# Kernel tuning notes

Hardware: AMD Instinct MI355X
Metric: run time of the kernel (lower is better)

Reference implementation:

```python
import jax, jax.numpy as jnp
import numpy as np

B, S, HID = 1, 2048, 2048
H, NOPE, ROPE, VDIM = 16, 128, 64, 128
QR, KVR = 1536, 512
IH, ID = 16, 128
TOPK = 512
THETA = 10000.0
EPS = 1e-6
SCALE = (NOPE + ROPE) ** -0.5
NEG = -1e9


def _cos_sin(s, dim, dtype):
    inv = 1.0 / (THETA ** (np.arange(0, dim, 2, dtype=np.float32) / dim))
    t = np.arange(s, dtype=np.float32)
    f = np.outer(t, inv)
    emb = np.concatenate([f, f], -1)
    return jnp.asarray(np.cos(emb), dtype), jnp.asarray(np.sin(emb), dtype)


def _rope(x, cos, sin):
    # x: [b,s,h,d]; cos/sin: [s,d]; NeoX-style rotate_half
    x1, x2 = jnp.split(x, 2, axis=-1)
    rot = jnp.concatenate([-x2, x1], axis=-1)
    return x * cos[None, :, None, :] + rot * sin[None, :, None, :]


def _rmsnorm(x, w):
    v = jnp.mean(x.astype(jnp.float32) ** 2, -1, keepdims=True)
    return (x.astype(jnp.float32) * jax.lax.rsqrt(v + EPS)).astype(x.dtype) * w


def _layernorm(x, w, b):
    m = jnp.mean(x, -1, keepdims=True)
    v = jnp.var(x, -1, keepdims=True)
    return (x - m) * jax.lax.rsqrt(v + EPS) * w + b


def setup_inputs() -> dict:
    key = jax.random.key(0)
    ks = jax.random.split(key, 12)
    g = lambda k, shp: jax.random.normal(k, shp, jnp.float32) * 0.02
    return {
        'hidden_states': jax.random.normal(ks[0], (B, S, HID), jnp.float32),
        'q_a_w': g(ks[1], (QR, HID)),
        'q_a_ln_w': jnp.ones((QR,), jnp.float32),
        'q_b_w': g(ks[2], (H * (NOPE + ROPE), QR)),
        'kv_a_w': g(ks[3], (KVR + ROPE, HID)),
        'kv_a_ln_w': jnp.ones((KVR,), jnp.float32),
        'kv_b_w': g(ks[4], (H * (NOPE + VDIM), KVR)),
        'o_w': g(ks[5], (HID, H * VDIM)),
        'idx_wq_b_w': g(ks[6], (IH * ID, QR)),
        'idx_wk_w': g(ks[7], (ID, HID)),
        'idx_kn_w': jnp.ones((ID,), jnp.float32),
        'idx_kn_b': jnp.zeros((ID,), jnp.float32),
        'idx_wproj_w': g(ks[8], (IH, HID)),
    }


def reference(hidden_states, q_a_w, q_a_ln_w, q_b_w, kv_a_w, kv_a_ln_w, kv_b_w, o_w,
              idx_wq_b_w, idx_wk_w, idx_kn_w, idx_kn_b, idx_wproj_w):
    b, s, _ = hidden_states.shape
    cos, sin = _cos_sin(s, ROPE, hidden_states.dtype)

    # --- MLA projections ---
    qr = _rmsnorm(hidden_states @ q_a_w.T, q_a_ln_w)                 # [b,s,QR]
    q = (qr @ q_b_w.T).reshape(b, s, H, NOPE + ROPE)
    q_nope, q_pe = q[..., :NOPE], q[..., NOPE:]
    q_pe = _rope(q_pe, cos, sin)
    ckv = hidden_states @ kv_a_w.T                                   # [b,s,KVR+ROPE]
    c_kv, k_pe = ckv[..., :KVR], ckv[..., KVR:]
    k_pe = _rope(k_pe[:, :, None, :], cos, sin)                      # [b,s,1,ROPE]
    kv = (_rmsnorm(c_kv, kv_a_ln_w) @ kv_b_w.T).reshape(b, s, H, NOPE + VDIM)
    k_nope, v = kv[..., :NOPE], kv[..., NOPE:]

    # --- DSA indexer: per-token importance scores ---
    iq = (qr @ idx_wq_b_w.T).reshape(b, s, IH, ID)
    iq = jnp.concatenate([_rope(iq[..., :ROPE], cos, sin), iq[..., ROPE:]], -1)
    ik = _layernorm(hidden_states @ idx_wk_w.T, idx_kn_w, idx_kn_b)  # [b,s,ID]
    ik_pe = _rope(ik[:, :, None, :ROPE], cos, sin)[:, :, 0, :]
    ik = jnp.concatenate([ik_pe, ik[..., ROPE:]], -1)
    iw = (hidden_states @ idx_wproj_w.T) * (IH ** -0.5)              # [b,s,IH]
    idx_scores = jnp.einsum('bqh,bhqk->bqk', iw,
                            jax.nn.relu(jnp.einsum('bqhd,bkd->bhqk', iq, ik)))
    causal = jnp.tril(jnp.ones((s, s), bool))
    idx_scores = jnp.where(causal[None], idx_scores, -jnp.inf)
    _, top_idx = jax.lax.top_k(idx_scores, TOPK)                     # [b,s,TOPK]
    bi = jnp.arange(b)[:, None, None]
    qi = jnp.arange(s)[None, :, None]
    keep = jnp.zeros((b, s, s), bool).at[bi, qi, top_idx].set(True)
    allowed = keep & causal[None]                                    # [b,s,s]

    # --- sparse top-k attention (top-k mask to -inf before softmax) ---
    qh = jnp.concatenate([q_nope, q_pe], -1)                         # [b,s,H,192]
    kh = jnp.concatenate([k_nope, jnp.broadcast_to(k_pe, (b, s, H, ROPE))], -1)
    scores = jnp.einsum('bqhd,bkhd->bhqk', qh, kh) * SCALE
    scores = jnp.where(allowed[:, None], scores, NEG)
    attn = jax.nn.softmax(scores, -1)
    out = jnp.einsum('bhqk,bkhd->bqhd', attn, v).reshape(b, s, H * VDIM)
    return out @ o_w.T
```

## Files before the change

kernel.cpp:

```cpp
#include <hip/hip_runtime.h>
#include <hip/hip_bf16.h>
#include <math.h>

#define SEQ 2048
#define HIDD 2048
#define QRANK 1536
#define KVRANK 512
#define TOPK 512
#define EPSF 1e-6f
#define SCALE_ATTN 0.07216878364870323f
#define NCAT 1680

typedef __attribute__((ext_vector_type(8))) short short8v;
typedef __attribute__((ext_vector_type(4))) short short4v;
typedef __attribute__((ext_vector_type(4))) float f32x4;

__device__ inline unsigned short f2bf(float f) {
    unsigned u = __float_as_uint(f);
    unsigned r = (u + 0x7FFFu + ((u >> 16) & 1u)) >> 16;
    return (unsigned short)r;
}
__device__ inline float bf2f(unsigned short b) {
    return __uint_as_float(((unsigned)b) << 16);
}
__device__ inline void split2(float x, unsigned short& h, unsigned short& l) {
    h = f2bf(x);
    l = f2bf(x - bf2f(h));
}

__device__ inline short4v ds_read_tr16(const void* p) {
#if __has_builtin(__builtin_amdgcn_ds_read_tr16_b64)
    return __builtin_amdgcn_ds_read_tr16_b64((short4v*)p);
#else
    const unsigned short* u = (const unsigned short*)p;
    short4v r;
    r[0] = (short)u[0]; r[1] = (short)u[16]; r[2] = (short)u[32]; r[3] = (short)u[48];
    return r;
#endif
}

__global__ __launch_bounds__(256) void cvt_bf16_4_kernel(
    const float* __restrict__ a, int na4, const float* __restrict__ b, int nb4,
    const float* __restrict__ c, int nc4, const float* __restrict__ d, int nd4,
    unsigned short* __restrict__ oa, unsigned short* __restrict__ ob,
    unsigned short* __restrict__ oc, unsigned short* __restrict__ od,
    float* __restrict__ cos_t, float* __restrict__ sin_t)
{
    if (blockIdx.x < SEQ && threadIdx.x < 32) {
        int s = blockIdx.x, i = threadIdx.x;
        double inv = pow(10000.0, -((double)(2 * i)) / 64.0);
        double f = (double)s * inv;
        cos_t[s * 32 + i] = (float)cos(f);
        sin_t[s * 32 + i] = (float)sin(f);
    }
    int total = na4 + nb4 + nc4 + nd4;
    for (int i = blockIdx.x * 256 + threadIdx.x; i < total; i += gridDim.x * 256) {
        const float* src; unsigned short* dst; int j = i;
        if (j < na4) { src = a; dst = oa; }
        else if ((j -= na4) < nb4) { src = b; dst = ob; }
        else if ((j -= nb4) < nc4) { src = c; dst = oc; }
        else { j -= nc4; src = d; dst = od; }
        float4 v = ((const float4*)src)[j];
        ushort4 o;
        o.x = f2bf(v.x); o.y = f2bf(v.y); o.z = f2bf(v.z); o.w = f2bf(v.w);
        ((ushort4*)dst)[j] = o;
    }
}

__global__ __launch_bounds__(256) void cvt_split3_kernel(
    const float* __restrict__ hidden, const float* __restrict__ q_a_w,
    const float* __restrict__ idx_wk_w, const float* __restrict__ idx_wproj_w,
    const float* __restrict__ wq,
    unsigned short* __restrict__ hidh, unsigned short* __restrict__ hidl,
    unsigned short* __restrict__ catwh, unsigned short* __restrict__ catwl,
    unsigned short* __restrict__ wqh, unsigned short* __restrict__ wql)
{
    const int nhid4 = HIDD * HIDD / 4;
    const int ncat4 = NCAT * HIDD / 4;
    const int nwq4  = HIDD * QRANK / 4;
    int total = nhid4 + ncat4 + nwq4;
    for (int i = blockIdx.x * 256 + threadIdx.x; i < total; i += gridDim.x * 256) {
        int j = i;
        const float4* s4;
        unsigned short *dh, *dl;
        float scale = 1.f;
        if (j < nhid4) {
            s4 = (const float4*)hidden + j; dh = hidh; dl = hidl;
        } else if ((j -= nhid4) < ncat4) {
            int row = (j * 4) >> 11;
            dh = catwh; dl = catwl;
            if (row < 1536) s4 = (const float4*)q_a_w + j;
            else if (row < 1664) s4 = (const float4*)idx_wk_w + (j - 1536 * 512);
            else { s4 = (const float4*)idx_wproj_w + (j - 1664 * 512); scale = 0.25f; }
        } else {
            j -= ncat4;
            s4 = (const float4*)wq + j; dh = wqh; dl = wql;
        }
        float4 v = *s4;
        float xs[4] = {v.x * scale, v.y * scale, v.z * scale, v.w * scale};
        ushort4 oh, ol;
        unsigned short h2, l2;
        split2(xs[0], h2, l2); oh.x = h2; ol.x = l2;
        split2(xs[1], h2, l2); oh.y = h2; ol.y = l2;
        split2(xs[2], h2, l2); oh.z = h2; ol.z = l2;
        split2(xs[3], h2, l2); oh.w = h2; ol.w = l2;
        ((ushort4*)dh)[j] = oh;
        ((ushort4*)dl)[j] = ol;
    }
}

__global__ __launch_bounds__(256) void wkt_kernel(const float* __restrict__ kvb,
                                                  unsigned short* __restrict__ wkt) {
    __shared__ float t[128][129];
    int h = blockIdx.x, n0 = blockIdx.y * 128;
    int tid = threadIdx.x;
    for (int it = tid; it < 128 * 32; it += 256) {
        int d = it >> 5, c4 = it & 31;
        float4 v = *(const float4*)(kvb + ((size_t)(h * 256 + d)) * 512 + n0 + c4 * 4);
        t[d][c4 * 4 + 0] = v.x; t[d][c4 * 4 + 1] = v.y;
        t[d][c4 * 4 + 2] = v.z; t[d][c4 * 4 + 3] = v.w;
    }
    __syncthreads();
    for (int it = tid; it < 128 * 32; it += 256) {
        int n = it >> 5, dc = it & 31;
        ushort4 o;
        o.x = f2bf(t[dc * 4 + 0][n]); o.y = f2bf(t[dc * 4 + 1][n]);
        o.z = f2bf(t[dc * 4 + 2][n]); o.w = f2bf(t[dc * 4 + 3][n]);
        *(ushort4*)(wkt + ((size_t)h * 512 + n0 + n) * 128 + dc * 4) = o;
    }
}

__global__ __launch_bounds__(256) void gemm_cat_split_kernel(
    const float* __restrict__ hidden, const float* __restrict__ q_a_w,
    const float* __restrict__ idx_wk_w, const float* __restrict__ idx_wproj_w,
    const unsigned short* __restrict__ hidh, const unsigned short* __restrict__ hidl,
    const unsigned short* __restrict__ catwh, const unsigned short* __restrict__ catwl,
    float* __restrict__ ccat)
{
    __shared__ __align__(16) unsigned short Ah[128 * 32], Al[128 * 32];
    __shared__ __align__(16) unsigned short Bh[128 * 32], Bl[128 * 32];
    int tid = threadIdx.x;
    int l = tid & 63, w = tid >> 6;
    int wr = w >> 1, wc = w & 1;
    int m0 = blockIdx.x * 128, n0 = blockIdx.y * 128;
    const bool pre = (hidh != nullptr);
    f32x4 acc[4][4] = {};
    for (int k0 = 0; k0 < HIDD; k0 += 32) {
        __syncthreads();
#pragma unroll
        for (int i = 0; i < 2; ++i) {
            int idx = tid + i * 256;
            int r = idx >> 2, cc = idx & 3;
            int sw = cc ^ (r & 3);
            int gb = n0 + r; if (gb > NCAT - 1) gb = NCAT - 1;
            if (pre) {
                size_t abase = (size_t)(m0 + r) * HIDD + k0 + cc * 8;
                *(short8v*)&Ah[r * 32 + sw * 8] = *(const short8v*)(hidh + abase);
                *(short8v*)&Al[r * 32 + sw * 8] = *(const short8v*)(hidl + abase);
                size_t bbase = (size_t)gb * HIDD + k0 + cc * 8;
                *(short8v*)&Bh[r * 32 + sw * 8] = *(const short8v*)(catwh + bbase);
                *(short8v*)&Bl[r * 32 + sw * 8] = *(const short8v*)(catwl + bbase);
            } else {
                {
                    const float* src = hidden + (size_t)(m0 + r) * HIDD + k0 + cc * 8;
                    float4 f0 = *(const float4*)src, f1 = *(const float4*)(src + 4);
                    float xs[8] = {f0.x, f0.y, f0.z, f0.w, f1.x, f1.y, f1.z, f1.w};
                    short8v dh, dl;
#pragma unroll
                    for (int e = 0; e < 8; ++e) {
                        unsigned short hh, ll; split2(xs[e], hh, ll);
                        dh[e] = (short)hh; dl[e] = (short)ll;
                    }
                    *(short8v*)&Ah[r * 32 + sw * 8] = dh;
                    *(short8v*)&Al[r * 32 + sw * 8] = dl;
                }
                {
                    float scale = 1.f;
                    const float* src;
                    if (gb < 1536) src = q_a_w + (size_t)gb * HIDD;
                    else if (gb < 1664) src = idx_wk_w + (size_t)(gb - 1536) * HIDD;
                    else { src = idx_wproj_w + (size_t)(gb - 1664) * HIDD; scale = 0.25f; }
                    src += k0 + cc * 8;
                    float4 f0 = *(const float4*)src, f1 = *(const float4*)(src + 4);
                    float xs[8] = {f0.x, f0.y, f0.z, f0.w, f1.x, f1.y, f1.z, f1.w};
                    short8v dh, dl;
#pragma unroll
                    for (int e = 0; e < 8; ++e) {
                        unsigned short hh, ll; split2(xs[e] * scale, hh, ll);
                        dh[e] = (short)hh; dl[e] = (short)ll;
                    }
                    *(short8v*)&Bh[r * 32 + sw * 8] = dh;
                    *(short8v*)&Bl[r * 32 + sw * 8] = dl;
                }
            }
        }
        __syncthreads();
        short8v avh[4], avl[4];
#pragma unroll
        for (int mt = 0; mt < 4; ++mt) {
            int row = wr * 64 + mt * 16 + (l & 15);
            int ch = (l >> 4) ^ (row & 3);
            avh[mt] = *(const short8v*)&Ah[row * 32 + ch * 8];
            avl[mt] = *(const short8v*)&Al[row * 32 + ch * 8];
        }
#pragma unroll
        for (int nt = 0; nt < 4; ++nt) {
            int row = wc * 64 + nt * 16 + (l & 15);
            int ch = (l >> 4) ^ (row & 3);
            short8v bvh = *(const short8v*)&Bh[row * 32 + ch * 8];
            short8v bvl = *(const short8v*)&Bl[row * 32 + ch * 8];
#pragma unroll
            for (int mt = 0; mt < 4; ++mt) {
                acc[mt][nt] = __builtin_amdgcn_mfma_f32_16x16x32_bf16(avh[mt], bvh, acc[mt][nt], 0, 0, 0);
                acc[mt][nt] = __builtin_amdgcn_mfma_f32_16x16x32_bf16(avh[mt], bvl, acc[mt][nt], 0, 0, 0);
                acc[mt][nt] = __builtin_amdgcn_mfma_f32_16x16x32_bf16(avl[mt], bvh, acc[mt][nt], 0, 0, 0);
            }
        }
    }
#pragma unroll
    for (int mt = 0; mt < 4; ++mt)
#pragma unroll
        for (int nt = 0; nt < 4; ++nt)
#pragma unroll
            for (int i = 0; i < 4; ++i) {
                int gm = m0 + wr * 64 + mt * 16 + (l >> 4) * 4 + i;
                int gn = n0 + wc * 64 + nt * 16 + (l & 15);
                if (gn < NCAT) ccat[(size_t)gm * NCAT + gn] = acc[mt][nt][i];
            }
}

__global__ __launch_bounds__(256) void gemm_iq_split_kernel(
    const float* __restrict__ qr, const float* __restrict__ wq,
    const unsigned short* __restrict__ qrh, const unsigned short* __restrict__ qrl,
    const unsigned short* __restrict__ wqh, const unsigned short* __restrict__ wql,
    const float* __restrict__ cos_t, const float* __restrict__ sin_t,
    unsigned short* __restrict__ iqh, unsigned short* __restrict__ iql)
{
    __shared__ __align__(16) unsigned short Ah[128 * 32], Al[128 * 32];
    __shared__ __align__(16) unsigned short Bh[128 * 32], Bl[128 * 32];
    int tid = threadIdx.x;
    int l = tid & 63, w = tid >> 6;
    int wr = w >> 1, wc = w & 1;
    int m0 = blockIdx.x * 128, n0 = blockIdx.y * 128;
    int hh_ = blockIdx.y;
    const bool pre = (wqh != nullptr);
    f32x4 acc[4][4] = {};
    for (int k0 = 0; k0 < QRANK; k0 += 32) {
        __syncthreads();
#pragma unroll
        for (int i = 0; i < 2; ++i) {
            int idx = tid + i * 256;
            int r = idx >> 2, cc = idx & 3;
            int sw = cc ^ (r & 3);
            if (pre) {
                size_t abase = (size_t)(m0 + r) * QRANK + k0 + cc * 8;
                *(short8v*)&Ah[r * 32 + sw * 8] = *(const short8v*)(qrh + abase);
                *(short8v*)&Al[r * 32 + sw * 8] = *(const short8v*)(qrl + abase);
                size_t bbase = (size_t)(n0 + r) * QRANK + k0 + cc * 8;
                *(short8v*)&Bh[r * 32 + sw * 8] = *(const short8v*)(wqh + bbase);
                *(short8v*)&Bl[r * 32 + sw * 8] = *(const short8v*)(wql + bbase);
            } else {
                {
                    const float* src = qr + (size_t)(m0 + r) * QRANK + k0 + cc * 8;
                    float4 f0 = *(const float4*)src, f1 = *(const float4*)(src + 4);
                    float xs[8] = {f0.x, f0.y, f0.z, f0.w, f1.x, f1.y, f1.z, f1.w};
                    short8v dh, dl;
#pragma unroll
                    for (int e = 0; e < 8; ++e) {
                        unsigned short h2, l2; split2(xs[e], h2, l2);
                        dh[e] = (short)h2; dl[e] = (short)l2;
                    }
                    *(short8v*)&Ah[r * 32 + sw * 8] = dh;
                    *(short8v*)&Al[r * 32 + sw * 8] = dl;
                }
                {
                    const float* src = wq + (size_t)(n0 + r) * QRANK + k0 + cc * 8;
                    float4 f0 = *(const float4*)src, f1 = *(const float4*)(src + 4);
                    float xs[8] = {f0.x, f0.y, f0.z, f0.w, f1.x, f1.y, f1.z, f1.w};
                    short8v dh, dl;
#pragma unroll
                    for (int e = 0; e < 8; ++e) {
                        unsigned short h2, l2; split2(xs[e], h2, l2);
                        dh[e] = (short)h2; dl[e] = (short)l2;
                    }
                    *(short8v*)&Bh[r * 32 + sw * 8] = dh;
                    *(short8v*)&Bl[r * 32 + sw * 8] = dl;
                }
            }
        }
        __syncthreads();
        short8v avh[4], avl[4];
#pragma unroll
        for (int mt = 0; mt < 4; ++mt) {
            int row = wr * 64 + mt * 16 + (l & 15);
            int ch = (l >> 4) ^ (row & 3);
            avh[mt] = *(const short8v*)&Ah[row * 32 + ch * 8];
            avl[mt] = *(const short8v*)&Al[row * 32 + ch * 8];
        }
#pragma unroll
        for (int nt = 0; nt < 4; ++nt) {
            int row = wc * 64 + nt * 16 + (l & 15);
            int ch = (l >> 4) ^ (row & 3);
            short8v bvh = *(const short8v*)&Bh[row * 32 + ch * 8];
            short8v bvl = *(const short8v*)&Bl[row * 32 + ch * 8];
#pragma unroll
            for (int mt = 0; mt < 4; ++mt) {
                acc[mt][nt] = __builtin_amdgcn_mfma_f32_16x16x32_bf16(avh[mt], bvh, acc[mt][nt], 0, 0, 0);
                acc[mt][nt] = __builtin_amdgcn_mfma_f32_16x16x32_bf16(avh[mt], bvl, acc[mt][nt], 0, 0, 0);
                acc[mt][nt] = __builtin_amdgcn_mfma_f32_16x16x32_bf16(avl[mt], bvh, acc[mt][nt], 0, 0, 0);
            }
        }
    }
    if (wc == 0) {
#pragma unroll
        for (int mt = 0; mt < 4; ++mt)
#pragma unroll
            for (int nt = 0; nt < 2; ++nt)
#pragma unroll
                for (int i = 0; i < 4; ++i) {
                    int q = m0 + wr * 64 + mt * 16 + (l >> 4) * 4 + i;
                    int dd = nt * 16 + (l & 15);
                    float c = cos_t[q * 32 + dd], s = sin_t[q * 32 + dd];
                    float x1 = acc[mt][nt][i], x2 = acc[mt][nt + 2][i];
                    acc[mt][nt][i] = x1 * c - x2 * s;
                    acc[mt][nt + 2][i] = x2 * c + x1 * s;
                }
    }
#pragma unroll
    for (int mt = 0; mt < 4; ++mt)
#pragma unroll
        for (int nt = 0; nt < 4; ++nt)
#pragma unroll
            for (int i = 0; i < 4; ++i) {
                int q = m0 + wr * 64 + mt * 16 + (l >> 4) * 4 + i;
                int d = wc * 64 + nt * 16 + (l & 15);
                size_t idx = ((size_t)q * 16 + hh_) * 128 + d;
                unsigned short h2, l2; split2(acc[mt][nt][i], h2, l2);
                iqh[idx] = h2; iql[idx] = l2;
            }
}

template <typename TA, typename TC>
__global__ __launch_bounds__(256) void mfma_nt_kernel(
    const TA* __restrict__ A, const unsigned short* __restrict__ B, TC* __restrict__ C,
    int M, int N, int K, int lda, int ldb, int ldc, long ab, long bb, long cb,
    const float* __restrict__ cos_t, const float* __restrict__ sin_t, int rope_mode,
    unsigned short* __restrict__ qnope)
{
    __shared__ __align__(16) unsigned short Asl[128 * 32];
    __shared__ __align__(16) unsigned short Bsl[128 * 32];
    int z = blockIdx.z;
    const TA* Az = A + (size_t)z * ab;
    const unsigned short* Bz = B + (size_t)z * bb;
    TC* Cz = C + (size_t)z * cb;
    int tid = threadIdx.x;
    int l = tid & 63, w = tid >> 6;
    int wr = w >> 1, wc = w & 1;
    int m0 = blockIdx.x * 128, n0 = blockIdx.y * 128;
    f32x4 acc[4][4] = {};

    for (int k0 = 0; k0 < K; k0 += 32) {
        __syncthreads();
#pragma unroll
        for (int i = 0; i < 2; ++i) {
            int idx = tid + i * 256;
            int r = idx >> 2, cc = idx & 3;
            int sw = cc ^ (r & 3);
            {
                short8v d;
                const TA* src = Az + (size_t)(m0 + r) * lda + k0 + cc * 8;
                if constexpr (sizeof(TA) == 2) {
                    d = *(const short8v*)src;
                } else {
                    float4 f0 = *(const float4*)src;
                    float4 f1 = *(const float4*)(src + 4);
                    d[0] = (short)f2bf(f0.x); d[1] = (short)f2bf(f0.y);
                    d[2] = (short)f2bf(f0.z); d[3] = (short)f2bf(f0.w);
                    d[4] = (short)f2bf(f1.x); d[5] = (short)f2bf(f1.y);
                    d[6] = (short)f2bf(f1.z); d[7] = (short)f2bf(f1.w);
                }
                *(short8v*)&Asl[r * 32 + sw * 8] = d;
            }
            {
                int gb = n0 + r; if (gb > N - 1) gb = N - 1;
                short8v d = *(const short8v*)(Bz + (size_t)gb * ldb + k0 + cc * 8);
                *(short8v*)&Bsl[r * 32 + sw * 8] = d;
            }
        }
        __syncthreads();
        short8v av[4], bv[4];
#pragma unroll
        for (int mt = 0; mt < 4; ++mt) {
            int row = wr * 64 + mt * 16 + (l & 15);
            int ch = (l >> 4) ^ (row & 3);
            av[mt] = *(const short8v*)&Asl[row * 32 + ch * 8];
        }
#pragma unroll
        for (int nt = 0; nt < 4; ++nt) {
            int row = wc * 64 + nt * 16 + (l & 15);
            int ch = (l >> 4) ^ (row & 3);
            bv[nt] = *(const short8v*)&Bsl[row * 32 + ch * 8];
        }
#pragma unroll
        for (int mt = 0; mt < 4; ++mt)
#pragma unroll
            for (int nt = 0; nt < 4; ++nt)
                acc[mt][nt] = __builtin_amdgcn_mfma_f32_16x16x32_bf16(av[mt], bv[nt], acc[mt][nt], 0, 0, 0);
    }
    if (rope_mode) {
        int gcol64 = (n0 >> 6) + wc;
        bool dorope = (rope_mode == 1) ? ((gcol64 % 3) == 2) : (gcol64 == 8);
        if (dorope) {
#pragma unroll
            for (int mt = 0; mt < 4; ++mt)
#pragma unroll
                for (int nt = 0; nt < 2; ++nt)
#pragma unroll
                    for (int i = 0; i < 4; ++i) {
                        int q = m0 + wr * 64 + mt * 16 + (l >> 4) * 4 + i;
                        int dd = nt * 16 + (l & 15);
                        float c = cos_t[q * 32 + dd], sn = sin_t[q * 32 + dd];
                        float x1 = acc[mt][nt][i], x2 = acc[mt][nt + 2][i];
                        acc[mt][nt][i] = x1 * c - x2 * sn;
                        acc[mt][nt + 2][i] = x2 * c + x1 * sn;
                    }
        }
    }
#pragma unroll
    for (int mt = 0; mt < 4; ++mt) {
#pragma unroll
        for (int nt = 0; nt < 4; ++nt) {
#pragma unroll
            for (int i = 0; i < 4; ++i) {
                int gm = m0 + wr * 64 + mt * 16 + (l >> 4) * 4 + i;
                int gn = n0 + wc * 64 + nt * 16 + (l & 15);
                if (gn < N) {
                    float v = acc[mt][nt][i];
                    if constexpr (sizeof(TC) == 4) Cz[(size_t)gm * ldc + gn] = v;
                    else Cz[(size_t)gm * ldc + gn] = f2bf(v);
                    if (rope_mode == 1 && qnope) {
                        int gh = gn / 192, gr = gn - gh * 192;
                        if (gr < 128)
                            qnope[(size_t)gm * 2048 + gh * 128 + gr] = f2bf(v);
                    }
                }
            }
        }
    }
}

__global__ __launch_bounds__(256) void norms_fused_kernel(
    const float* __restrict__ ccat,
    const float* __restrict__ q_a_ln_w, float* __restrict__ qr_out,
    unsigned short* __restrict__ qr_bf, unsigned short* __restrict__ qr_lo,
    const float* __restrict__ ikn_w, const float* __restrict__ ikn_b,
    const float* __restrict__ cos_t, const float* __restrict__ sin_t,
    unsigned short* __restrict__ ikh, unsigned short* __restrict__ ikl)
{
    int blk = blockIdx.x, tid = threadIdx.x;
    if (blk < SEQ) {
        int row = blk;
        const float* x = ccat + (size_t)row * NCAT;
        float4 v[2];
        int cnt = 0;
        float ss = 0.f;
        const int nf4 = QRANK >> 2;
        for (int i = tid; i < nf4; i += 256) {
            float4 t = *(const float4*)(x + i * 4);
            v[cnt++] = t;
            ss += t.x * t.x + t.y * t.y + t.z * t.z + t.w * t.w;
        }
#pragma unroll
        for (int m = 32; m; m >>= 1) ss += __shfl_xor(ss, m);
        __shared__ float red[8];
        if ((tid & 63) == 0) red[tid >> 6] = ss;
        __syncthreads();
        if (tid == 0) {
            float s = red[0] + red[1] + red[2] + red[3];
            red[4] = rsqrtf(s / (float)QRANK + EPSF);
        }
        __syncthreads();
        float scale = red[4];
        cnt = 0;
        for (int i = tid; i < nf4; i += 256) {
            float4 t = v[cnt++];
            float4 wv = *(const float4*)(q_a_ln_w + i * 4);
            float4 o;
            o.x = t.x * scale * wv.x; o.y = t.y * scale * wv.y;
            o.z = t.z * scale * wv.z; o.w = t.w * scale * wv.w;
            *(float4*)(qr_out + (size_t)row * QRANK + i * 4) = o;
            ushort4 ob;
            ob.x = f2bf(o.x); ob.y = f2bf(o.y); ob.z = f2bf(o.z); ob.w = f2bf(o.w);
            *(ushort4*)(qr_bf + (size_t)row * QRANK + i * 4) = ob;
            if (qr_lo) {
                ushort4 ol;
                ol.x = f2bf(o.x - bf2f(ob.x)); ol.y = f2bf(o.y - bf2f(ob.y));
                ol.z = f2bf(o.z - bf2f(ob.z)); ol.w = f2bf(o.w - bf2f(ob.w));
                *(ushort4*)(qr_lo + (size_t)row * QRANK + i * 4) = ol;
            }
        }
    } else {
        if (tid >= 64) return;
        int row = blk - SEQ;
        const float* x = ccat + (size_t)row * NCAT + 1536;
        float x0 = x[tid], x1 = x[tid + 64];
        float s = x0 + x1, ss = x0 * x0 + x1 * x1;
#pragma unroll
        for (int m = 32; m; m >>= 1) { s += __shfl_xor(s, m); ss += __shfl_xor(ss, m); }
        float mean = s * (1.f / 128.f);
        float var = ss * (1.f / 128.f) - mean * mean;
        float r = rsqrtf(var + EPSF);
        float n0 = (x0 - mean) * r * ikn_w[tid] + ikn_b[tid];
        float n1 = (x1 - mean) * r * ikn_w[tid + 64] + ikn_b[tid + 64];
        float c = cos_t[row * 32 + (tid & 31)], sn = sin_t[row * 32 + (tid & 31)];
        float other = __shfl_xor(n0, 32);
        float r0 = (tid < 32) ? (n0 * c - other * sn) : (n0 * c + other * sn);
        unsigned short h2, l2;
        split2(r0, h2, l2);
        ikh[(size_t)row * 128 + tid] = h2; ikl[(size_t)row * 128 + tid] = l2;
        split2(n1, h2, l2);
        ikh[(size_t)row * 128 + 64 + tid] = h2; ikl[(size_t)row * 128 + 64 + tid] = l2;
    }
}

__global__ __launch_bounds__(256) void rmsnorm_khg_kernel(
    const float* __restrict__ ckv, const float* __restrict__ w,
    unsigned short* __restrict__ khg)
{
    int row = blockIdx.x, tid = threadIdx.x;
    const float* x = ckv + (size_t)row * 576;
    float4 v = make_float4(0.f, 0.f, 0.f, 0.f);
    float ss = 0.f;
    if (tid < 128) {
        v = *(const float4*)(x + tid * 4);
        ss = v.x * v.x + v.y * v.y + v.z * v.z + v.w * v.w;
    }
#pragma unroll
    for (int mm = 32; mm; mm >>= 1) ss += __shfl_xor(ss, mm);
    __shared__ float red[8];
    if ((tid & 63) == 0) red[tid >> 6] = ss;
    __syncthreads();
    if (tid == 0) red[4] = rsqrtf((red[0] + red[1] + red[2] + red[3]) * (1.f / 512.f) + EPSF);
    __syncthreads();
    float scale = red[4];
    if (tid < 128) {
        float4 wv = *(const float4*)(w + tid * 4);
        ushort4 ob;
        ob.x = f2bf(v.x * scale * wv.x); ob.y = f2bf(v.y * scale * wv.y);
        ob.z = f2bf(v.z * scale * wv.z); ob.w = f2bf(v.w * scale * wv.w);
        *(ushort4*)(khg + (size_t)row * 576 + tid * 4) = ob;
    } else if (tid < 192) {
        khg[(size_t)row * 576 + 512 + (tid - 128)] = f2bf(x[512 + tid - 128]);
    }
}

__global__ __launch_bounds__(256) void idx_scores_mfma_kernel(
    const unsigned short* __restrict__ iqh, const unsigned short* __restrict__ iql,
    const unsigned short* __restrict__ ikh, const unsigned short* __restrict__ ikl,
    const float* __restrict__ iwsrc, int iw_stride,
    float* __restrict__ scores)
{
    int q0 = blockIdx.x * 64, k0 = blockIdx.y * 64;
    int tid = threadIdx.x;
    if (k0 > q0 + 63) {
        for (int t = tid; t < 64 * 64; t += 256) {
            int r = t >> 6, c = t & 63;
            scores[(size_t)(q0 + r) * SEQ + k0 + c] = -INFINITY;
        }
        return;
    }
    __shared__ float iws[64][16];
    int l = tid & 63, w = tid >> 6;
    {
        int r = tid >> 2, c = tid & 3;
        *(float4*)&iws[r][c * 4] = *(const float4*)(iwsrc + (size_t)(q0 + r) * iw_stride + c * 4);
    }
    __syncthreads();
    short8v bhr[4][4], blr[4][4];
#pragma unroll
    for (int nt = 0; nt < 4; ++nt)
#pragma unroll
        for (int ks = 0; ks < 4; ++ks) {
            size_t base = (size_t)(k0 + nt * 16 + (l & 15)) * 128 + ks * 32 + (l >> 4) * 8;
            bhr[nt][ks] = *(const short8v*)(ikh + base);
            blr[nt][ks] = *(const short8v*)(ikl + base);
        }
    f32x4 acc[4] = {};
    const int arow = q0 + w * 16 + (l & 15);
    for (int h = 0; h < 16; ++h) {
        f32x4 dot[4] = {};
#pragma unroll
        for (int ks = 0; ks < 4; ++ks) {
            size_t abase = ((size_t)arow * 16 + h) * 128 + ks * 32 + (l >> 4) * 8;
            short8v ah = *(const short8v*)(iqh + abase);
            short8v al = *(const short8v*)(iql + abase);
#pragma unroll
            for (int nt = 0; nt < 4; ++nt) {
                dot[nt] = __builtin_amdgcn_mfma_f32_16x16x32_bf16(ah, bhr[nt][ks], dot[nt], 0, 0, 0);
                dot[nt] = __builtin_amdgcn_mfma_f32_16x16x32_bf16(ah, blr[nt][ks], dot[nt], 0, 0, 0);
                dot[nt] = __builtin_amdgcn_mfma_f32_16x16x32_bf16(al, bhr[nt][ks], dot[nt], 0, 0, 0);
            }
        }
#pragma unroll
        for (int nt = 0; nt < 4; ++nt)
#pragma unroll
            for (int i = 0; i < 4; ++i) {
                float wv = iws[w * 16 + (l >> 4) * 4 + i][h];
                acc[nt][i] += wv * fmaxf(dot[nt][i], 0.f);
            }
    }
#pragma unroll
    for (int nt = 0; nt < 4; ++nt)
#pragma unroll
        for (int i = 0; i < 4; ++i) {
            int q = q0 + w * 16 + (l >> 4) * 4 + i;
            int k = k0 + nt * 16 + (l & 15);
            scores[(size_t)q * SEQ + k] = (k <= q) ? acc[nt][i] : -INFINITY;
        }
}

__global__ __launch_bounds__(1024) void topk_kernel(
    const float* __restrict__ scores, int* __restrict__ sel)
{
    int qi = blockIdx.x, tid = threadIdx.x;
    __shared__ unsigned long long keys[2048];
    const float* srow = scores + (size_t)qi * SEQ;
#pragma unroll
    for (int r = 0; r < 2; ++r) {
        int k = tid + r * 1024;
        unsigned u = __float_as_uint(srow[k]);
        unsigned mv = (u & 0x80000000u) ? ~u : (u | 0x80000000u);
        keys[k] = ((unsigned long long)mv << 32) | (unsigned)(2047 - k);
    }
    for (int ksz = 2; ksz <= 2048; ksz <<= 1) {
        for (int j = ksz >> 1; j > 0; j >>= 1) {
            __syncthreads();
#pragma unroll 1
            for (int r = 0; r < 2; ++r) {
                int i = tid + r * 1024;
                int ixj = i ^ j;
                if (ixj > i) {
                    unsigned long long a = keys[i], b = keys[ixj];
                    bool dir = ((i & ksz) == 0);
                    if ((a < b) == dir) { keys[i] = b; keys[ixj] = a; }
                }
            }
        }
    }
    __syncthreads();
    if (tid < TOPK) {
        int k = 2047 - (int)(keys[tid] & 0xFFFFFFFFu);
        sel[(size_t)qi * TOPK + tid] = (tid <= qi) ? k : -1;
    }
}

__global__ __launch_bounds__(256) void attn_mfma_kernel(
    const unsigned short* __restrict__ qabs,
    const float* __restrict__ qsrc,
    const unsigned short* __restrict__ khg,
    const int* __restrict__ sel,
    unsigned short* __restrict__ ocomp)
{
    __shared__ __align__(16) char smem[77824];
    unsigned short* plds = (unsigned short*)(smem + 74752);
    float* smax = (float*)(smem + 77312);
    float* ssum = (float*)(smem + 77568);

    const int qi = blockIdx.x;
    const int tid = threadIdx.x;
    const int l = tid & 63, w = tid >> 6;
    const int lg = l >> 4, lr = l & 15;
    const int nv = min(TOPK, qi + 1);
    const int ntile = (nv + 63) >> 6;
    const int krow = w * 16 + lr;

    const int ck = tid >> 6, cc = tid & 63;
    const int pk = tid >> 3, pc = tid & 7;
    const int* selrow = sel + (size_t)qi * TOPK;

    short8v aq[18];
    {
        const unsigned short* qa = qabs + ((size_t)qi * 16 + lr) * 512 + lg * 8;
#pragma unroll
        for (int ks = 0; ks < 16; ++ks)
            aq[ks] = *(const short8v*)(qa + ks * 32);
        const float* qp = qsrc + (size_t)qi * 3072 + lr * 192 + 128 + lg * 8;
#pragma unroll
        for (int ks = 0; ks < 2; ++ks) {
            float4 f0 = *(const float4*)(qp + ks * 32);
            float4 f1 = *(const float4*)(qp + ks * 32 + 4);
            short8v d;
            d[0] = (short)f2bf(f0.x); d[1] = (short)f2bf(f0.y);
            d[2] = (short)f2bf(f0.z); d[3] = (short)f2bf(f0.w);
            d[4] = (short)f2bf(f1.x); d[5] = (short)f2bf(f1.y);
            d[6] = (short)f2bf(f1.z); d[7] = (short)f2bf(f1.w);
            aq[16 + ks] = d;
        }
    }

    const int sbase = krow * 32 + (lg >> 1) * 2080 + (lg & 1) * 16;
    const int vboff = w * 16640 + lg * 256 + lr * 2;

    float m[4] = {-1e30f, -1e30f, -1e30f, -1e30f};
    float lsum[4] = {0.f, 0.f, 0.f, 0.f};
    f32x4 oacc[8] = {};

    for (int t = 0; t < ntile; ++t) {
        const int j0 = t * 64;
        __syncthreads();
#pragma unroll
        for (int j = 0; j < 16; ++j) {
            int sv = selrow[j0 + ck + 4 * j];
            if (sv < 0) sv = 0;
            short8v v = *(const short8v*)(khg + (size_t)sv * 576 + cc * 8);
            *(short8v*)(smem + (cc >> 1) * 2080 + (ck + 4 * j) * 32 + (cc & 1) * 16) = v;
        }
#pragma unroll
        for (int j = 0; j < 2; ++j) {
            int sv = selrow[j0 + pk + 32 * j];
            if (sv < 0) sv = 0;
            short8v v = *(const short8v*)(khg + (size_t)sv * 576 + 512 + pc * 8);
            int key = pk + 32 * j;
            *(short8v*)(smem + 66560 + ((key * 128 + pc * 16) ^ ((key & 7) << 4))) = v;
        }
        __syncthreads();
        f32x4 s = {};
        __builtin_amdgcn_s_setprio(1);
#pragma unroll
        for (int ks = 0; ks < 16; ++ks) {
            short8v b = *(const short8v*)(smem + sbase + ks * 4160);
            s = __builtin_amdgcn_mfma_f32_16x16x32_bf16(aq[ks], b, s, 0, 0, 0);
        }
#pragma unroll
        for (int ks = 0; ks < 2; ++ks) {
            short8v b = *(const short8v*)(smem + 66560 +
                ((krow * 128 + ks * 64 + lg * 16) ^ ((krow & 7) << 4)));
            s = __builtin_amdgcn_mfma_f32_16x16x32_bf16(aq[16 + ks], b, s, 0, 0, 0);
        }
        __builtin_amdgcn_s_setprio(0);
        bool kvalid = (j0 + krow) < nv;
#pragma unroll
        for (int i = 0; i < 4; ++i)
            s[i] = kvalid ? s[i] * SCALE_ATTN : -1e30f;
        float tm[4];
#pragma unroll
        for (int i = 0; i < 4; ++i) tm[i] = s[i];
#pragma unroll
        for (int sh = 1; sh < 16; sh <<= 1)
#pragma unroll
            for (int i = 0; i < 4; ++i) tm[i] = fmaxf(tm[i], __shfl_xor(tm[i], sh));
        if (lr == 0) *(float4*)&smax[w * 16 + lg * 4] = make_float4(tm[0], tm[1], tm[2], tm[3]);
        __syncthreads();
        float mn[4], scl[4];
#pragma unroll
        for (int i = 0; i < 4; ++i) {
            int h = lg * 4 + i;
            float tmax = fmaxf(fmaxf(smax[h], smax[16 + h]), fmaxf(smax[32 + h], smax[48 + h]));
            mn[i] = fmaxf(m[i], tmax);
            scl[i] = __expf(m[i] - mn[i]);
            m[i] = mn[i];
        }
        float p[4], rs[4];
#pragma unroll
        for (int i = 0; i < 4; ++i) { p[i] = __expf(s[i] - mn[i]); rs[i] = p[i]; }
#pragma unroll
        for (int sh = 1; sh < 16; sh <<= 1)
#pragma unroll
            for (int i = 0; i < 4; ++i) rs[i] += __shfl_xor(rs[i], sh);
        if (lr == 0) *(float4*)&ssum[w * 16 + lg * 4] = make_float4(rs[0], rs[1], rs[2], rs[3]);
#pragma unroll
        for (int i = 0; i < 4; ++i)
            plds[(lg * 4 + i) * 80 + krow] = f2bf(p[i]);
        __syncthreads();
#pragma unroll
        for (int i = 0; i < 4; ++i) {
            int h = lg * 4 + i;
            float ts = ssum[h] + ssum[16 + h] + ssum[32 + h] + ssum[48 + h];
            lsum[i] = lsum[i] * scl[i] + ts;
        }
#pragma unroll
        for (int nt = 0; nt < 8; ++nt)
#pragma unroll
            for (int i = 0; i < 4; ++i) oacc[nt][i] *= scl[i];
        __builtin_amdgcn_s_setprio(1);
#pragma unroll
        for (int kb = 0; kb < 2; ++kb) {
            short8v af = *(const short8v*)&plds[lr * 80 + kb * 32 + lg * 8];
#pragma unroll
            for (int nt = 0; nt < 8; ++nt) {
                const char* a = smem + vboff + kb * 1024 + nt * 2080;
                short4v t0 = ds_read_tr16(a);
                short4v t1 = ds_read_tr16(a + 128);
                short8v bf = __builtin_shufflevector(t0, t1, 0, 1, 2, 3, 4, 5, 6, 7);
                oacc[nt] = __builtin_amdgcn_mfma_f32_16x16x32_bf16(af, bf, oacc[nt], 0, 0, 0);
            }
        }
        __builtin_amdgcn_s_setprio(0);
    }
    float inv[4];
#pragma unroll
    for (int i = 0; i < 4; ++i) inv[i] = 1.f / lsum[i];
    unsigned short* ob = ocomp + (size_t)qi * 16 * 512;
#pragma unroll
    for (int nt = 0; nt < 8; ++nt) {
        int d = w * 128 + nt * 16 + lr;
#pragma unroll
        for (int i = 0; i < 4; ++i) {
            int h = lg * 4 + i;
            ob[h * 512 + d] = f2bf(oacc[nt][i] * inv[i]);
        }
    }
}

extern "C" void kernel_launch(void* const* d_in, const int* in_sizes, int n_in,
                              void* d_out, int out_size, void* d_ws, size_t ws_size,
                              hipStream_t stream) {
    (void)in_sizes; (void)n_in; (void)out_size;
    const float* hidden      = (const float*)d_in[0];
    const float* q_a_w       = (const float*)d_in[1];
    const float* q_a_ln_w    = (const float*)d_in[2];
    const float* q_b_w       = (const float*)d_in[3];
    const float* kv_a_w      = (const float*)d_in[4];
    const float* kv_a_ln_w   = (const float*)d_in[5];
    const float* kv_b_w      = (const float*)d_in[6];
    const float* o_w         = (const float*)d_in[7];
    const float* idx_wq_b_w  = (const float*)d_in[8];
    const float* idx_wk_w    = (const float*)d_in[9];
    const float* idx_kn_w    = (const float*)d_in[10];
    const float* idx_kn_b    = (const float*)d_in[11];
    const float* idx_wproj_w = (const float*)d_in[12];
    float* out = (float*)d_out;

    char* ws = (char*)d_ws;
    size_t off = 0;
    auto alloc = [&](size_t nbytes) -> void* {
        void* p = ws + off;
        off = (off + nbytes + 255) & ~(size_t)255;
        return p;
    };
    float* cos_t = (float*)alloc((size_t)SEQ * 32 * 4);
    float* sin_t = (float*)alloc((size_t)SEQ * 32 * 4);
    float* qbuf  = (float*)alloc((size_t)SEQ * 3072 * 4);
    float* ckv   = (float*)alloc((size_t)SEQ * 576 * 4);
    int*   sel   = (int*)alloc((size_t)SEQ * TOPK * 4);
    unsigned short* khg      = (unsigned short*)alloc((size_t)SEQ * 576 * 2);
    unsigned short* attno_bf = (unsigned short*)alloc((size_t)SEQ * 2048 * 2);
    unsigned short* qr_bf    = (unsigned short*)alloc((size_t)SEQ * QRANK * 2);
    unsigned short* q_b_bf   = (unsigned short*)alloc((size_t)3072 * QRANK * 2);
    unsigned short* kv_a_bf  = (unsigned short*)alloc((size_t)576 * HIDD * 2);
    unsigned short* o_w_bf   = (unsigned short*)alloc((size_t)HIDD * 2048 * 2);
    unsigned short* kv_b_bf  = (unsigned short*)alloc((size_t)4096 * 512 * 2);
    unsigned short* wkt      = (unsigned short*)alloc((size_t)16 * 512 * 128 * 2);
    unsigned short* qnope_bf = attno_bf;
    size_t mark = off;
    float* qr    = (float*)alloc((size_t)SEQ * QRANK * 4);
    float* ccat  = (float*)alloc((size_t)SEQ * NCAT * 4);
    float* scores = (float*)alloc((size_t)SEQ * SEQ * 4);
    unsigned short* iqh = (unsigned short*)alloc((size_t)SEQ * 2048 * 2);
    unsigned short* iql = (unsigned short*)alloc((size_t)SEQ * 2048 * 2);
    unsigned short* ikh = (unsigned short*)alloc((size_t)SEQ * 128 * 2);
    unsigned short* ikl = (unsigned short*)alloc((size_t)SEQ * 128 * 2);
    unsigned short* hidh  = (unsigned short*)alloc((size_t)HIDD * HIDD * 2);
    unsigned short* hidl  = (unsigned short*)alloc((size_t)HIDD * HIDD * 2);
    unsigned short* catwh = (unsigned short*)alloc((size_t)NCAT * HIDD * 2);
    unsigned short* catwl = (unsigned short*)alloc((size_t)NCAT * HIDD * 2);
    unsigned short* wqh   = (unsigned short*)alloc((size_t)HIDD * QRANK * 2);
    unsigned short* wql   = (unsigned short*)alloc((size_t)HIDD * QRANK * 2);
    unsigned short* qr_l  = (unsigned short*)alloc((size_t)SEQ * QRANK * 2);
    bool fast = (off <= ws_size);
    if (!fast) {
        hidh = hidl = catwh = catwl = wqh = wql = qr_l = nullptr;
    }
    off = mark;
    unsigned short* qabsb = (unsigned short*)alloc((size_t)SEQ * 16 * 512 * 2);
    unsigned short* ocomp = (unsigned short*)alloc((size_t)SEQ * 16 * 512 * 2);

    cvt_bf16_4_kernel<<<2048, 256, 0, stream>>>(
        q_b_w, 3072 * QRANK / 4, kv_a_w, 576 * HIDD / 4,
        o_w, HIDD * 2048 / 4, kv_b_w, 4096 * 512 / 4,
        q_b_bf, kv_a_bf, o_w_bf, kv_b_bf, cos_t, sin_t);
    wkt_kernel<<<dim3(16, 4), 256, 0, stream>>>(kv_b_w, wkt);
    if (fast)
        cvt_split3_kernel<<<2048, 256, 0, stream>>>(
            hidden, q_a_w, idx_wk_w, idx_wproj_w, idx_wq_b_w,
            hidh, hidl, catwh, catwl, wqh, wql);

    gemm_cat_split_kernel<<<dim3(16, 14), 256, 0, stream>>>(
        hidden, q_a_w, idx_wk_w, idx_wproj_w, hidh, hidl, catwh, catwl, ccat);

    norms_fused_kernel<<<2 * SEQ, 256, 0, stream>>>(
        ccat, q_a_ln_w, qr, qr_bf, qr_l, idx_kn_w, idx_kn_b, cos_t, sin_t, ikh, ikl);

    mfma_nt_kernel<unsigned short, float><<<dim3(16, 24, 1), 256, 0, stream>>>(
        qr_bf, q_b_bf, qbuf, SEQ, 3072, QRANK, QRANK, QRANK, 3072, 0L, 0L, 0L,
        cos_t, sin_t, 1, qnope_bf);

    mfma_nt_kernel<float, float><<<dim3(16, 5, 1), 256, 0, stream>>>(
        hidden, kv_a_bf, ckv, SEQ, 576, HIDD, HIDD, HIDD, 576, 0L, 0L, 0L,
        cos_t, sin_t, 2, nullptr);
    rmsnorm_khg_kernel<<<SEQ, 256, 0, stream>>>(ckv, kv_a_ln_w, khg);

    gemm_iq_split_kernel<<<dim3(16, 16), 256, 0, stream>>>(
        qr, idx_wq_b_w, qr_bf, qr_l, wqh, wql, cos_t, sin_t, iqh, iql);

    idx_scores_mfma_kernel<<<dim3(32, 32), 256, 0, stream>>>(iqh, iql, ikh, ikl, ccat + 1664, NCAT, scores);
    topk_kernel<<<SEQ, 1024, 0, stream>>>(scores, sel);

    mfma_nt_kernel<unsigned short, unsigned short><<<dim3(16, 4, 16), 256, 0, stream>>>(
        qnope_bf, wkt, qabsb, SEQ, 512, 128, 2048, 128, 16 * 512,
        128L, 512L * 128L, 512L, nullptr, nullptr, 0, nullptr);

    attn_mfma_kernel<<<SEQ, 256, 0, stream>>>(qabsb, qbuf, khg, sel, ocomp);

    mfma_nt_kernel<unsigned short, unsigned short><<<dim3(16, 1, 16), 256, 0, stream>>>(
        ocomp, kv_b_bf + (size_t)128 * 512, attno_bf, SEQ, 128, 512,
        16 * 512, 512, 2048, 512L, 256L * 512L, 128L, nullptr, nullptr, 0, nullptr);

    mfma_nt_kernel<unsigned short, float><<<dim3(16, 16, 1), 256, 0, stream>>>(
        attno_bf, o_w_bf, out, SEQ, HIDD, 2048, 2048, 2048, HIDD, 0L, 0L, 0L,
        nullptr, nullptr, 0, nullptr);
}
```

Baseline: 801.9 us.

## Stage indexer K and per-head Q tiles through swizzled LDS; skip redundant q-nope stores

The indexer score kernel now loads the K tile (hi/lo bf16 parts) into XOR-swizzled shared memory with coalesced row loads. Each head's Q tile is also staged through shared memory, so operands no longer come from strided per-lane global loads. This adds two block barriers per head and 64KB of LDS per block, which may lower occupancy. Separately, the projection GEMM epilogue no longer writes q-nope columns to the main output when they are already written to the qnope buffer, which cuts redundant global stores.

New measurement: 807.5 us. Within noise of the previous version (+0.7%).

```diff
diff --git a/kernel.cpp b/kernel.cpp
--- a/kernel.cpp
+++ b/kernel.cpp
@@ -436,12 +436,15 @@
                 int gn = n0 + wc * 64 + nt * 16 + (l & 15);
                 if (gn < N) {
                     float v = acc[mt][nt][i];
-                    if constexpr (sizeof(TC) == 4) Cz[(size_t)gm * ldc + gn] = v;
-                    else Cz[(size_t)gm * ldc + gn] = f2bf(v);
                     if (rope_mode == 1 && qnope) {
                         int gh = gn / 192, gr = gn - gh * 192;
                         if (gr < 128)
                             qnope[(size_t)gm * 2048 + gh * 128 + gr] = f2bf(v);
+                        else
+                            Cz[(size_t)gm * ldc + gn] = v;
+                    } else {
+                        if constexpr (sizeof(TC) == 4) Cz[(size_t)gm * ldc + gn] = v;
+                        else Cz[(size_t)gm * ldc + gn] = f2bf(v);
                     }
                 }
             }
@@ -569,8 +572,16 @@
         }
         return;
     }
+    __shared__ __align__(16) unsigned short skh[64 * 128], skl[64 * 128];
+    __shared__ __align__(16) unsigned short sqh[64 * 128], sql[64 * 128];
     __shared__ float iws[64][16];
     int l = tid & 63, w = tid >> 6;
+    for (int it = tid; it < 64 * 16; it += 256) {
+        int r = it >> 4, c = it & 15;
+        int sw = c ^ (r & 15);
+        *(short8v*)&skh[r * 128 + sw * 8] = *(const short8v*)(ikh + (size_t)(k0 + r) * 128 + c * 8);
+        *(short8v*)&skl[r * 128 + sw * 8] = *(const short8v*)(ikl + (size_t)(k0 + r) * 128 + c * 8);
+    }
     {
         int r = tid >> 2, c = tid & 3;
         *(float4*)&iws[r][c * 4] = *(const float4*)(iwsrc + (size_t)(q0 + r) * iw_stride + c * 4);
@@ -581,19 +592,29 @@
     for (int nt = 0; nt < 4; ++nt)
 #pragma unroll
         for (int ks = 0; ks < 4; ++ks) {
-            size_t base = (size_t)(k0 + nt * 16 + (l & 15)) * 128 + ks * 32 + (l >> 4) * 8;
-            bhr[nt][ks] = *(const short8v*)(ikh + base);
-            blr[nt][ks] = *(const short8v*)(ikl + base);
+            int brow = nt * 16 + (l & 15);
+            int bch = ((l >> 4) + ks * 4) ^ (brow & 15);
+            bhr[nt][ks] = *(const short8v*)&skh[brow * 128 + bch * 8];
+            blr[nt][ks] = *(const short8v*)&skl[brow * 128 + bch * 8];
         }
     f32x4 acc[4] = {};
-    const int arow = q0 + w * 16 + (l & 15);
     for (int h = 0; h < 16; ++h) {
+        __syncthreads();
+        for (int it = tid; it < 64 * 16; it += 256) {
+            int r = it >> 4, c = it & 15;
+            int sw = c ^ (r & 15);
+            size_t base = ((size_t)(q0 + r) * 16 + h) * 128 + c * 8;
+            *(short8v*)&sqh[r * 128 + sw * 8] = *(const short8v*)(iqh + base);
+            *(short8v*)&sql[r * 128 + sw * 8] = *(const short8v*)(iql + base);
+        }
+        __syncthreads();
         f32x4 dot[4] = {};
 #pragma unroll
         for (int ks = 0; ks < 4; ++ks) {
-            size_t abase = ((size_t)arow * 16 + h) * 128 + ks * 32 + (l >> 4) * 8;
-            short8v ah = *(const short8v*)(iqh + abase);
-            short8v al = *(const short8v*)(iql + abase);
+            int arow = w * 16 + (l & 15);
+            int ach = ((l >> 4) + ks * 4) ^ (arow & 15);
+            short8v ah = *(const short8v*)&sqh[arow * 128 + ach * 8];
+            short8v al = *(const short8v*)&sql[arow * 128 + ach * 8];
 #pragma unroll
             for (int nt = 0; nt < 4; ++nt) {
                 dot[nt] = __builtin_amdgcn_mfma_f32_16x16x32_bf16(ah, bhr[nt][ks], dot[nt], 0, 0, 0);
```
